# Kernel optimization log

Measured on AMD Instinct MI355X. Metric: run time of the kernel, lower is better.

Reference implementation:

```python
import jax, jax.numpy as jnp
import numpy as np

BOND_TOL = 0.4
CLASH_TOL = 1.5
IDEAL_CA_CA = 3.8
EPS = 1e-08


def setup_inputs() -> dict:
    key = jax.random.key(0)
    k1, _ = jax.random.split(key)
    B, L = 8, 2048
    positions = jax.random.normal(k1, (B, L, 3), dtype=jnp.float32) * 10.0
    mask = jnp.ones((B, L), dtype=jnp.float32)
    return {"positions": positions, "mask": mask}


def reference(positions, mask):
    # positions: [B, L, 3] CA coordinates; mask: [B, L]
    L = positions.shape[1]
    ca = positions
    ca_mask = mask

    # --- bond term: consecutive CA-CA distances ---
    ca_diff = ca[:, 1:] - ca[:, :-1]                       # [B, L-1, 3]
    ca_dist = jnp.sqrt(jnp.sum(ca_diff ** 2, axis=-1) + EPS)
    bond_violation = jax.nn.relu(jnp.abs(ca_dist - IDEAL_CA_CA) - BOND_TOL)
    bond_mask = ca_mask[:, 1:] * ca_mask[:, :-1]
    bond_loss = jnp.sum(bond_violation * bond_mask) / (jnp.sum(bond_mask) + EPS)

    # --- clash term: all-pairs distances, non-bonded (|i-j| > 2) ---
    all_diff = ca[:, :, None, :] - ca[:, None, :, :]       # [B, L, L, 3]
    all_dist = jnp.sqrt(jnp.sum(all_diff ** 2, axis=-1) + EPS)  # [B, L, L]
    idx = jnp.arange(L)
    seq_sep = jnp.abs(idx[None, :] - idx[:, None])         # [L, L]
    non_bonded = (seq_sep > 2).astype(ca.dtype)
    clash_violation = jax.nn.relu(CLASH_TOL - all_dist)
    pair_mask = ca_mask[:, :, None] * ca_mask[:, None, :] * non_bonded[None]
    clash_loss = jnp.sum(clash_violation * pair_mask) / (jnp.sum(pair_mask) + EPS)

    total = bond_loss + clash_loss
    # stacked: [bond_loss, clash_loss, total_violation]
    return jnp.stack([bond_loss, clash_loss, total])
```

## Files before the change

kernel.cpp:

```cpp
#include <hip/hip_runtime.h>

#define TPB 256
#define RPB 16
#define SEQ_L 2048
#define JPT (SEQ_L / TPB)
#define NBATCH 8
#define NBLOCKS (NBATCH * (SEQ_L / RPB))

static constexpr float kBondTol  = 0.4f;
static constexpr float kClashTol = 1.5f;
static constexpr float kIdeal    = 3.8f;
static constexpr float kEps      = 1e-8f;
static constexpr float kThresh2  = 2.25f;

__device__ __forceinline__ float wred(float v) {
#pragma unroll
  for (int o = 32; o > 0; o >>= 1) v += __shfl_down(v, o, 64);
  return v;
}

__global__ __launch_bounds__(TPB, 4) void viol_main(
    const float* __restrict__ pos,
    const float* __restrict__ mask,
    float4* __restrict__ partial) {
  __shared__ float4 s[SEQ_L];
  __shared__ float  redm[TPB / 64];
  __shared__ float  red4[TPB / 64][4];

  const int u = blockIdx.x >> 3;
  const int b = blockIdx.x & 7;
  const int v = u >> 5, rr = u & 31;
  int tile;
  if      (v == 0) tile = 2 * rr;
  else if (v == 1) tile = 127 - 2 * rr;
  else if (v == 2) tile = 2 * rr + 1;
  else             tile = 126 - 2 * rr;
  const int i0 = tile << 4;

  const float* pb = pos  + (size_t)b * SEQ_L * 3;
  const float* mb = mask + (size_t)b * SEQ_L;

  float mpart = 0.f;
  for (int idx = threadIdx.x; idx < SEQ_L; idx += TPB) {
    float x = pb[3 * idx + 0];
    float y = pb[3 * idx + 1];
    float z = pb[3 * idx + 2];
    float m = mb[idx];
    s[idx] = make_float4(x, y, z, m);
    mpart += m;
  }
  mpart = wred(mpart);
  const int wid  = threadIdx.x >> 6;
  const int lane = threadIdx.x & 63;
  if (lane == 0) redm[wid] = mpart;
  __syncthreads();
  const float msum = redm[0] + redm[1] + redm[2] + redm[3];

  float px[RPB], py[RPB], pz[RPB], pw[RPB], accr[RPB];
#pragma unroll
  for (int r = 0; r < RPB; ++r) {
    float4 p = s[i0 + r];
    px[r] = p.x; py[r] = p.y; pz[r] = p.z; pw[r] = p.w;
    accr[r] = 0.f;
  }

  const int k0 = i0 >> 8;
  {
    const int j = threadIdx.x + (k0 << 8);
    const float4 pj = s[j];
#pragma unroll
    for (int r = 0; r < RPB; ++r) {
      const int i = i0 + r;
      float dx = pj.x - px[r];
      float dy = pj.y - py[r];
      float dz = pj.z - pz[r];
      float d2 = fmaf(dx, dx, fmaf(dy, dy, dz * dz));
      float dist = __builtin_amdgcn_sqrtf(d2 + kEps);
      float mw = (j > i) ? pj.w : 0.f;
      accr[r] = fmaf(fmaxf(kClashTol - dist, 0.f), mw, accr[r]);
    }
  }

#pragma unroll 2
  for (int k = k0 + 1; k < JPT; ++k) {
    float4 pj = s[threadIdx.x + (k << 8)];
    float d2r[RPB];
#pragma unroll
    for (int r = 0; r < RPB; ++r) {
      float dx = pj.x - px[r];
      float dy = pj.y - py[r];
      float dz = pj.z - pz[r];
      d2r[r] = fmaf(dx, dx, fmaf(dy, dy, dz * dz));
    }
    float mv = d2r[0];
#pragma unroll
    for (int r = 1; r < RPB; ++r) mv = fminf(mv, d2r[r]);
    if (__ballot(mv < kThresh2) != 0ull) {
#pragma unroll
      for (int r = 0; r < RPB; ++r) {
        float dist = __builtin_amdgcn_sqrtf(d2r[r] + kEps);
        accr[r] = fmaf(fmaxf(kClashTol - dist, 0.f), pj.w, accr[r]);
      }
    }
  }

  float cv = 0.f, pm = 0.f, bv = 0.f, bm = 0.f;
#pragma unroll
  for (int r = 0; r < RPB; ++r) cv = fmaf(pw[r], accr[r], cv);

  if (threadIdx.x < RPB) {
    const int i = i0 + threadIdx.x;
    const float4 pi = s[i];
    float nv = 0.f;
    const int jhi = (i + 2 > SEQ_L - 1) ? SEQ_L - 1 : i + 2;
    for (int j = i + 1; j <= jhi; ++j) {
      float4 pj = s[j];
      float dx = pj.x - pi.x;
      float dy = pj.y - pi.y;
      float dz = pj.z - pi.z;
      float dist = __builtin_amdgcn_sqrtf(dx * dx + dy * dy + dz * dz + kEps);
      nv += fmaxf(kClashTol - dist, 0.f) * pj.w;
    }
    cv -= pi.w * nv;

    float nm = 0.f;
    const int jlo = (i - 2 < 0) ? 0 : i - 2;
    for (int j = jlo; j <= jhi; ++j) nm += s[j].w;
    pm += pi.w * (msum - nm);

    if (i < SEQ_L - 1) {
      const float4 pj = s[i + 1];
      float dx = pj.x - pi.x;
      float dy = pj.y - pi.y;
      float dz = pj.z - pi.z;
      float dist = __builtin_amdgcn_sqrtf(dx * dx + dy * dy + dz * dz + kEps);
      float viol = fmaxf(fabsf(dist - kIdeal) - kBondTol, 0.f);
      bv += viol * pi.w * pj.w;
      bm += pi.w * pj.w;
    }
  }

  bv = wred(bv); bm = wred(bm); cv = wred(cv); pm = wred(pm);
  if (lane == 0) {
    red4[wid][0] = bv; red4[wid][1] = bm;
    red4[wid][2] = cv; red4[wid][3] = pm;
  }
  __syncthreads();
  if (threadIdx.x == 0) {
    float tbv = 0.f, tbm = 0.f, tcv = 0.f, tpm = 0.f;
#pragma unroll
    for (int w = 0; w < TPB / 64; ++w) {
      tbv += red4[w][0]; tbm += red4[w][1];
      tcv += red4[w][2]; tpm += red4[w][3];
    }
    partial[blockIdx.x] = make_float4(tbv, tbm, 2.f * tcv, tpm);
  }
}

__global__ __launch_bounds__(TPB) void viol_reduce(
    const float4* __restrict__ partial, float* __restrict__ out) {
  __shared__ float red4[TPB / 64][4];
  float bv = 0.f, bm = 0.f, cv = 0.f, pm = 0.f;
#pragma unroll
  for (int i = threadIdx.x; i < NBLOCKS; i += TPB) {
    float4 p = partial[i];
    bv += p.x; bm += p.y; cv += p.z; pm += p.w;
  }
  bv = wred(bv); bm = wred(bm); cv = wred(cv); pm = wred(pm);
  const int wid  = threadIdx.x >> 6;
  const int lane = threadIdx.x & 63;
  if (lane == 0) {
    red4[wid][0] = bv; red4[wid][1] = bm;
    red4[wid][2] = cv; red4[wid][3] = pm;
  }
  __syncthreads();
  if (threadIdx.x == 0) {
    float tbv = 0.f, tbm = 0.f, tcv = 0.f, tpm = 0.f;
#pragma unroll
    for (int w = 0; w < TPB / 64; ++w) {
      tbv += red4[w][0]; tbm += red4[w][1];
      tcv += red4[w][2]; tpm += red4[w][3];
    }
    float bond  = tbv / (tbm + kEps);
    float clash = tcv / (tpm + kEps);
    out[0] = bond;
    out[1] = clash;
    out[2] = bond + clash;
  }
}

extern "C" void kernel_launch(void* const* d_in, const int* in_sizes, int n_in,
                              void* d_out, int out_size, void* d_ws, size_t ws_size,
                              hipStream_t stream) {
  const float* pos  = (const float*)d_in[0];
  const float* mask = (const float*)d_in[1];
  float* out = (float*)d_out;
  float4* partial = (float4*)d_ws;

  viol_main<<<dim3(NBLOCKS), dim3(TPB), 0, stream>>>(pos, mask, partial);
  viol_reduce<<<dim3(1), dim3(TPB), 0, stream>>>(partial, out);
}
```

Before: 63.97 us.

## Process four balanced row tiles per 512-thread block to amortize staging

Each block now handles four 16-row tiles (r, 127-r, 63-r, 64+r) for one batch instead of one, with 512 threads and 512-column chunks. The grid shrinks from 1024 to 256 blocks. This cuts how many times each batch's full position array is loaded and staged into shared memory, and it balances the triangular work inside each block. In exchange there is less block-level parallelism (256 blocks on a 256-CU part) and the tile loop runs serially within a block. The final reduction kernel is simplified to one element per thread.

```diff
diff --git a/kernel.cpp b/kernel.cpp
--- a/kernel.cpp
+++ b/kernel.cpp
@@ -1,11 +1,13 @@
 #include <hip/hip_runtime.h>
 
-#define TPB 256
+#define TPB 512
 #define RPB 16
 #define SEQ_L 2048
-#define JPT (SEQ_L / TPB)
+#define CHUNK 512
+#define NCH (SEQ_L / CHUNK)
 #define NBATCH 8
-#define NBLOCKS (NBATCH * (SEQ_L / RPB))
+#define NBLOCKS 256
+#define NWAVE (TPB / 64)
 
 static constexpr float kBondTol  = 0.4f;
 static constexpr float kClashTol = 1.5f;
@@ -19,29 +21,26 @@
   return v;
 }
 
-__global__ __launch_bounds__(TPB, 4) void viol_main(
+__global__ __launch_bounds__(TPB, 2) void viol_main(
     const float* __restrict__ pos,
     const float* __restrict__ mask,
     float4* __restrict__ partial) {
   __shared__ float4 s[SEQ_L];
-  __shared__ float  redm[TPB / 64];
-  __shared__ float  red4[TPB / 64][4];
-
-  const int u = blockIdx.x >> 3;
+  __shared__ float  redm[NWAVE];
+  __shared__ float  red4[NWAVE][4];
+
   const int b = blockIdx.x & 7;
-  const int v = u >> 5, rr = u & 31;
-  int tile;
-  if      (v == 0) tile = 2 * rr;
-  else if (v == 1) tile = 127 - 2 * rr;
-  else if (v == 2) tile = 2 * rr + 1;
-  else             tile = 126 - 2 * rr;
-  const int i0 = tile << 4;
+  const int r = blockIdx.x >> 3;
+  int tiles[4];
+  tiles[0] = r; tiles[1] = 127 - r; tiles[2] = 63 - r; tiles[3] = 64 + r;
 
   const float* pb = pos  + (size_t)b * SEQ_L * 3;
   const float* mb = mask + (size_t)b * SEQ_L;
 
   float mpart = 0.f;
-  for (int idx = threadIdx.x; idx < SEQ_L; idx += TPB) {
+#pragma unroll
+  for (int it = 0; it < SEQ_L / TPB; ++it) {
+    int idx = threadIdx.x + it * TPB;
     float x = pb[3 * idx + 0];
     float y = pb[3 * idx + 1];
     float z = pb[3 * idx + 2];
@@ -54,62 +53,71 @@
   const int lane = threadIdx.x & 63;
   if (lane == 0) redm[wid] = mpart;
   __syncthreads();
-  const float msum = redm[0] + redm[1] + redm[2] + redm[3];
-
-  float px[RPB], py[RPB], pz[RPB], pw[RPB], accr[RPB];
-#pragma unroll
-  for (int r = 0; r < RPB; ++r) {
-    float4 p = s[i0 + r];
-    px[r] = p.x; py[r] = p.y; pz[r] = p.z; pw[r] = p.w;
-    accr[r] = 0.f;
-  }
-
-  const int k0 = i0 >> 8;
-  {
-    const int j = threadIdx.x + (k0 << 8);
-    const float4 pj = s[j];
-#pragma unroll
-    for (int r = 0; r < RPB; ++r) {
-      const int i = i0 + r;
-      float dx = pj.x - px[r];
-      float dy = pj.y - py[r];
-      float dz = pj.z - pz[r];
-      float d2 = fmaf(dx, dx, fmaf(dy, dy, dz * dz));
-      float dist = __builtin_amdgcn_sqrtf(d2 + kEps);
-      float mw = (j > i) ? pj.w : 0.f;
-      accr[r] = fmaf(fmaxf(kClashTol - dist, 0.f), mw, accr[r]);
-    }
-  }
+  float msum = 0.f;
+#pragma unroll
+  for (int w = 0; w < NWAVE; ++w) msum += redm[w];
+
+  float cv = 0.f, pm = 0.f, bv = 0.f, bm = 0.f;
+
+  for (int tt = 0; tt < 4; ++tt) {
+    const int i0 = tiles[tt] << 4;
+
+    float px[RPB], py[RPB], pz[RPB], pw[RPB], accr[RPB];
+#pragma unroll
+    for (int q = 0; q < RPB; ++q) {
+      float4 p = s[i0 + q];
+      px[q] = p.x; py[q] = p.y; pz[q] = p.z; pw[q] = p.w;
+      accr[q] = 0.f;
+    }
+
+    const int k0 = i0 >> 9;
+
+    {
+      const int j = threadIdx.x + (k0 << 9);
+      const float4 pj = s[j];
+#pragma unroll
+      for (int q = 0; q < RPB; ++q) {
+        const int i = i0 + q;
+        float dx = pj.x - px[q];
+        float dy = pj.y - py[q];
+        float dz = pj.z - pz[q];
+        float d2 = fmaf(dx, dx, fmaf(dy, dy, dz * dz));
+        float dist = __builtin_amdgcn_sqrtf(d2 + kEps);
+        float mw = (j > i) ? pj.w : 0.f;
+        accr[q] = fmaf(fmaxf(kClashTol - dist, 0.f), mw, accr[q]);
+      }
+    }
 
 #pragma unroll 2
-  for (int k = k0 + 1; k < JPT; ++k) {
-    float4 pj = s[threadIdx.x + (k << 8)];
-    float d2r[RPB];
-#pragma unroll
-    for (int r = 0; r < RPB; ++r) {
-      float dx = pj.x - px[r];
-      float dy = pj.y - py[r];
-      float dz = pj.z - pz[r];
-      d2r[r] = fmaf(dx, dx, fmaf(dy, dy, dz * dz));
-    }
-    float mv = d2r[0];
-#pragma unroll
-    for (int r = 1; r < RPB; ++r) mv = fminf(mv, d2r[r]);
-    if (__ballot(mv < kThresh2) != 0ull) {
-#pragma unroll
-      for (int r = 0; r < RPB; ++r) {
-        float dist = __builtin_amdgcn_sqrtf(d2r[r] + kEps);
-        accr[r] = fmaf(fmaxf(kClashTol - dist, 0.f), pj.w, accr[r]);
+    for (int k = k0 + 1; k < NCH; ++k) {
+      float4 pj = s[threadIdx.x + (k << 9)];
+      float d2r[RPB];
+#pragma unroll
+      for (int q = 0; q < RPB; ++q) {
+        float dx = pj.x - px[q];
+        float dy = pj.y - py[q];
+        float dz = pj.z - pz[q];
+        d2r[q] = fmaf(dx, dx, fmaf(dy, dy, dz * dz));
       }
-    }
-  }
-
-  float cv = 0.f, pm = 0.f, bv = 0.f, bm = 0.f;
-#pragma unroll
-  for (int r = 0; r < RPB; ++r) cv = fmaf(pw[r], accr[r], cv);
-
-  if (threadIdx.x < RPB) {
-    const int i = i0 + threadIdx.x;
+      float mv = d2r[0];
+#pragma unroll
+      for (int q = 1; q < RPB; ++q) mv = fminf(mv, d2r[q]);
+      if (__ballot(mv < kThresh2) != 0ull) {
+#pragma unroll
+        for (int q = 0; q < RPB; ++q) {
+          float dist = __builtin_amdgcn_sqrtf(d2r[q] + kEps);
+          accr[q] = fmaf(fmaxf(kClashTol - dist, 0.f), pj.w, accr[q]);
+        }
+      }
+    }
+
+#pragma unroll
+    for (int q = 0; q < RPB; ++q) cv = fmaf(pw[q], accr[q], cv);
+  }
+
+  if (threadIdx.x < 64) {
+    const int tile = tiles[threadIdx.x >> 4];
+    const int i = (tile << 4) + (threadIdx.x & 15);
     const float4 pi = s[i];
     float nv = 0.f;
     const int jhi = (i + 2 > SEQ_L - 1) ? SEQ_L - 1 : i + 2;
@@ -149,7 +157,7 @@
   if (threadIdx.x == 0) {
     float tbv = 0.f, tbm = 0.f, tcv = 0.f, tpm = 0.f;
 #pragma unroll
-    for (int w = 0; w < TPB / 64; ++w) {
+    for (int w = 0; w < NWAVE; ++w) {
       tbv += red4[w][0]; tbm += red4[w][1];
       tcv += red4[w][2]; tpm += red4[w][3];
     }
@@ -157,16 +165,11 @@
   }
 }
 
-__global__ __launch_bounds__(TPB) void viol_reduce(
+__global__ __launch_bounds__(256) void viol_reduce(
     const float4* __restrict__ partial, float* __restrict__ out) {
-  __shared__ float red4[TPB / 64][4];
-  float bv = 0.f, bm = 0.f, cv = 0.f, pm = 0.f;
-#pragma unroll
-  for (int i = threadIdx.x; i < NBLOCKS; i += TPB) {
-    float4 p = partial[i];
-    bv += p.x; bm += p.y; cv += p.z; pm += p.w;
-  }
-  bv = wred(bv); bm = wred(bm); cv = wred(cv); pm = wred(pm);
+  __shared__ float red4[4][4];
+  float4 p = partial[threadIdx.x];
+  float bv = wred(p.x), bm = wred(p.y), cv = wred(p.z), pm = wred(p.w);
   const int wid  = threadIdx.x >> 6;
   const int lane = threadIdx.x & 63;
   if (lane == 0) {
@@ -177,7 +180,7 @@
   if (threadIdx.x == 0) {
     float tbv = 0.f, tbm = 0.f, tcv = 0.f, tpm = 0.f;
 #pragma unroll
-    for (int w = 0; w < TPB / 64; ++w) {
+    for (int w = 0; w < 4; ++w) {
       tbv += red4[w][0]; tbm += red4[w][1];
       tcv += red4[w][2]; tpm += red4[w][3];
     }
@@ -198,5 +201,5 @@
   float4* partial = (float4*)d_ws;
 
   viol_main<<<dim3(NBLOCKS), dim3(TPB), 0, stream>>>(pos, mask, partial);
-  viol_reduce<<<dim3(1), dim3(TPB), 0, stream>>>(partial, out);
-}
+  viol_reduce<<<dim3(1), dim3(256), 0, stream>>>(partial, out);
+}
```

After: 71.43 us. 11.7% more time.
